# Kernel tuning notes

Hardware: AMD Instinct MI355X
Metric: run time of the kernel (lower is better)

The kernel has to match this reference:

```python
import jax, jax.numpy as jnp
import numpy as np


def setup_inputs() -> dict:
    key = jax.random.key(0)
    ks = jax.random.split(key, 6)
    N, D, B, K, O = 100000, 128, 20000, 32, 128
    features = jax.random.normal(ks[0], (N, D), dtype=jnp.float32)
    raw_features = jax.random.normal(ks[1], (N, D), dtype=jnp.float32)
    W1 = jax.random.normal(ks[2], (D, D), dtype=jnp.float32) * (1.0 / np.sqrt(D))
    b1 = jnp.zeros((D,), dtype=jnp.float32)
    Wn = jax.random.normal(ks[3], (2 * D, O), dtype=jnp.float32) * (1.0 / np.sqrt(2 * D))
    node = jax.random.randint(ks[4], (B, 1), 0, N, dtype=jnp.int64)
    neighbours = jax.random.randint(ks[5], (B, K), 0, N, dtype=jnp.int64)
    return {"features": features, "raw_features": raw_features, "W1": W1,
            "b1": b1, "Wn": Wn, "node": node, "neighbours": neighbours}


def reference(features, raw_features, W1, b1, Wn, node, neighbours):
    # Gather self and neighbor features (irregular access)
    node_feat = features[node[:, 0]]            # [B, D]
    neigh_feat = features[neighbours]           # [B, K, D]
    # Dense + relu applied per neighbor (the single dense layer in build())
    h = jax.nn.relu(jnp.einsum('bkd,de->bke', neigh_feat, W1) + b1)  # [B, K, D]
    # meanpooling over neighbors
    pooled = jnp.mean(h, axis=1)                # [B, D]
    # concat + matmul + relu activation
    out = jax.nn.relu(jnp.concatenate([node_feat, pooled], axis=-1) @ Wn)  # [B, O]
    return (out, raw_features)
```

## Files before the change

### kernel.cpp

```cpp
#include <hip/hip_runtime.h>
#include <hip/hip_bf16.h>
#include <stdint.h>

typedef __bf16 bf16x8 __attribute__((ext_vector_type(8)));
typedef float  f32x4  __attribute__((ext_vector_type(4)));
typedef float  f32x2  __attribute__((ext_vector_type(2)));

#define N_NODES 100000
#define DIM     128
#define B_BATCH 20000
#define K_NB    32
#define O_OUT   128

#define GLOAD16(g, l)  __builtin_amdgcn_global_load_lds(                        \
    (const __attribute__((address_space(1))) void*)(g),                         \
    (__attribute__((address_space(3))) void*)(l), 16, 0, 0)

__device__ inline float blo(uint32_t u) { return __uint_as_float(u << 16); }
__device__ inline float bhi(uint32_t u) { return __uint_as_float(u & 0xffff0000u); }

__global__ void prep_weights(const float* __restrict__ W1,
                             const float* __restrict__ Wn,
                             __bf16* __restrict__ W1f,
                             __bf16* __restrict__ Wnf) {
    int tid = blockIdx.x * blockDim.x + threadIdx.x;
    if (tid < 16384) {
        int e = tid & 7, l = (tid >> 3) & 63, ct = (tid >> 9) & 7, kt = tid >> 12;
        int r0 = l & 15, kg = l >> 4;
        W1f[tid] = (__bf16)W1[(kt * 32 + kg * 8 + e) * DIM + ct * 16 + r0];
    }
    int t2 = tid - 16384;
    if (t2 >= 0 && t2 < 32768) {
        int e = t2 & 7, l = (t2 >> 3) & 63, ct = (t2 >> 9) & 7, kt = t2 >> 12;
        int r0 = l & 15, kg = l >> 4;
        Wnf[t2] = (__bf16)Wn[(kt * 32 + kg * 8 + e) * O_OUT + ct * 16 + r0];
    }
}

__global__ __launch_bounds__(256, 2)
void gemm_h(const float* __restrict__ X, const __bf16* __restrict__ W1f,
            const float* __restrict__ b1, __bf16* __restrict__ H) {
    __shared__ char lds[65536];
    char* Xs = lds;
    char* Wf = lds + 32768;
    const int tid = threadIdx.x;
    const int lane = tid & 63, wave = tid >> 6;
    const int r0 = lane & 15, kg = lane >> 4;
    const long base = (long)blockIdx.x * 64;

#pragma unroll
    for (int i = 0; i < 8; ++i) {
        int chunk = i * 256 + wave * 64 + lane;
        int lrow = chunk >> 5;
        int coff = (chunk & 31) << 4;
        long grow = base + lrow; if (grow > N_NODES - 1) grow = N_NODES - 1;
        const char* g = (const char*)X + grow * 512 + (coff ^ ((lrow & 7) << 4));
        GLOAD16(g, Xs + chunk * 16);
    }
#pragma unroll
    for (int i = 0; i < 8; ++i) {
        int chunk = i * 256 + wave * 64 + lane;
        GLOAD16((const char*)W1f + chunk * 16, Wf + chunk * 16);
    }
    __syncthreads();

    f32x4 acc[8];
#pragma unroll
    for (int t = 0; t < 8; ++t) acc[t] = (f32x4)0.0f;

    const int row = wave * 16 + r0;
    const int swz = (r0 & 7) << 4;
#pragma unroll
    for (int kt = 0; kt < 4; ++kt) {
        const int c0 = kt * 128 + kg * 32;
        f32x4 a0 = *(const f32x4*)(Xs + row * 512 + (c0 ^ swz));
        f32x4 a1 = *(const f32x4*)(Xs + row * 512 + ((c0 + 16) ^ swz));
        bf16x8 af;
        af[0]=(__bf16)a0[0]; af[1]=(__bf16)a0[1]; af[2]=(__bf16)a0[2]; af[3]=(__bf16)a0[3];
        af[4]=(__bf16)a1[0]; af[5]=(__bf16)a1[1]; af[6]=(__bf16)a1[2]; af[7]=(__bf16)a1[3];
#pragma unroll
        for (int ct = 0; ct < 8; ++ct) {
            bf16x8 bf = *(const bf16x8*)(Wf + ((kt * 8 + ct) * 64 + lane) * 16);
            acc[ct] = __builtin_amdgcn_mfma_f32_16x16x32_bf16(af, bf, acc[ct], 0, 0, 0);
        }
    }

    const long orow_base = base + wave * 16 + kg * 4;
#pragma unroll
    for (int ct = 0; ct < 8; ++ct) {
        const int col = ct * 16 + r0;
        const float bias = b1[col];
#pragma unroll
        for (int r = 0; r < 4; ++r) {
            const long orow = orow_base + r;
            if (orow < N_NODES) {
                float v = acc[ct][r] + bias;
                H[orow * DIM + col] = (__bf16)(v > 0.f ? v : 0.f);
            }
        }
    }
}

__global__ __launch_bounds__(256)
void pool_concat(const __bf16* __restrict__ H, const float* __restrict__ X,
                 const int* __restrict__ node, const int* __restrict__ nb,
                 __bf16* __restrict__ Cc) {
    const int lane = threadIdx.x & 63, wave = threadIdx.x >> 6;
    const int b = blockIdx.x * 4 + wave;
    const int g = lane >> 4, c = lane & 15;
    const int swz = (b & 7) << 4;
    char* crow = (char*)Cc + (long)b * 512;

    const int ni = node[b];
    f32x2 nf = *(const f32x2*)(X + (long)ni * DIM + lane * 2);
    union { __bf16 h[2]; uint32_t u; } pk;
    pk.h[0] = (__bf16)nf[0]; pk.h[1] = (__bf16)nf[1];
    *(uint32_t*)(crow + ((lane * 4) ^ swz)) = pk.u;

    const int* nbp = nb + b * K_NB;
    int idx[8];
#pragma unroll
    for (int i = 0; i < 8; ++i) idx[i] = nbp[i * 4 + g];
    float s[8] = {0.f, 0.f, 0.f, 0.f, 0.f, 0.f, 0.f, 0.f};
#pragma unroll
    for (int i = 0; i < 8; ++i) {
        uint4 u = *(const uint4*)(H + (long)idx[i] * DIM + c * 8);
        s[0] += blo(u.x); s[1] += bhi(u.x);
        s[2] += blo(u.y); s[3] += bhi(u.y);
        s[4] += blo(u.z); s[5] += bhi(u.z);
        s[6] += blo(u.w); s[7] += bhi(u.w);
    }
#pragma unroll
    for (int e = 0; e < 8; ++e) {
        s[e] += __shfl_xor(s[e], 16);
        s[e] += __shfl_xor(s[e], 32);
    }
    if (g == 0) {
        union { __bf16 h[8]; uint4 u; } pq;
#pragma unroll
        for (int e = 0; e < 8; ++e) pq.h[e] = (__bf16)(s[e] * (1.0f / K_NB));
        *(uint4*)(crow + ((256 + c * 16) ^ swz)) = pq.u;
    }
}

__global__ __launch_bounds__(256, 2)
void gemm_out(const __bf16* __restrict__ Cc, const __bf16* __restrict__ Wnf,
              float* __restrict__ Out) {
    __shared__ char lds[65536];
    char* As = lds;
    char* Wb = lds + 32768;
    const int tid = threadIdx.x;
    const int lane = tid & 63, wave = tid >> 6;
    const int r0 = lane & 15, kg = lane >> 4;
    const long base = (long)blockIdx.x * 64;

#pragma unroll
    for (int i = 0; i < 8; ++i) {
        int chunk = i * 256 + wave * 64 + lane;
        int lrow = chunk >> 5;
        long grow = base + lrow; if (grow > B_BATCH - 1) grow = B_BATCH - 1;
        const char* g = (const char*)Cc + grow * 512 + ((chunk & 31) << 4);
        GLOAD16(g, As + chunk * 16);
    }
#pragma unroll
    for (int i = 0; i < 8; ++i) {
        int chunk = i * 256 + wave * 64 + lane;
        GLOAD16((const char*)Wnf + chunk * 16, Wb + chunk * 16);
    }
    __syncthreads();

    f32x4 acc[8];
#pragma unroll
    for (int t = 0; t < 8; ++t) acc[t] = (f32x4)0.0f;

    const int row = wave * 16 + r0;
    const int swz = (r0 & 7) << 4;
#pragma unroll
    for (int kt = 0; kt < 4; ++kt) {
        bf16x8 af = *(const bf16x8*)(As + row * 512 + ((kt * 64 + kg * 16) ^ swz));
#pragma unroll
        for (int ct = 0; ct < 8; ++ct) {
            bf16x8 bf = *(const bf16x8*)(Wb + ((kt * 8 + ct) * 64 + lane) * 16);
            acc[ct] = __builtin_amdgcn_mfma_f32_16x16x32_bf16(af, bf, acc[ct], 0, 0, 0);
        }
    }
    __syncthreads();
#pragma unroll
    for (int i = 0; i < 8; ++i) {
        int chunk = i * 256 + wave * 64 + lane;
        GLOAD16((const char*)Wnf + 32768 + chunk * 16, Wb + chunk * 16);
    }
    __syncthreads();
#pragma unroll
    for (int kt = 4; kt < 8; ++kt) {
        bf16x8 af = *(const bf16x8*)(As + row * 512 + ((kt * 64 + kg * 16) ^ swz));
#pragma unroll
        for (int ct = 0; ct < 8; ++ct) {
            bf16x8 bf = *(const bf16x8*)(Wb + (((kt - 4) * 8 + ct) * 64 + lane) * 16);
            acc[ct] = __builtin_amdgcn_mfma_f32_16x16x32_bf16(af, bf, acc[ct], 0, 0, 0);
        }
    }

    const long orow_base = base + wave * 16 + kg * 4;
#pragma unroll
    for (int ct = 0; ct < 8; ++ct) {
        const int col = ct * 16 + r0;
#pragma unroll
        for (int r = 0; r < 4; ++r) {
            const long orow = orow_base + r;
            if (orow < B_BATCH) {
                float v = acc[ct][r];
                Out[orow * O_OUT + col] = v > 0.f ? v : 0.f;
            }
        }
    }
}

__global__ __launch_bounds__(256)
void copy_raw(const float4* __restrict__ src, float4* __restrict__ dst, int n4) {
    int i = blockIdx.x * blockDim.x + threadIdx.x;
    const int stride = gridDim.x * blockDim.x;
    for (; i < n4; i += stride) dst[i] = src[i];
}

extern "C" void kernel_launch(void* const* d_in, const int* in_sizes, int n_in,
                              void* d_out, int out_size, void* d_ws, size_t ws_size,
                              hipStream_t stream) {
    const float* features = (const float*)d_in[0];
    const float* raw      = (const float*)d_in[1];
    const float* W1       = (const float*)d_in[2];
    const float* b1       = (const float*)d_in[3];
    const float* Wn       = (const float*)d_in[4];
    const int*   node     = (const int*)d_in[5];
    const int*   nb       = (const int*)d_in[6];
    float* out = (float*)d_out;

    char* ws = (char*)d_ws;
    __bf16* H   = (__bf16*)ws;
    __bf16* W1f = (__bf16*)(ws + 25600000);
    __bf16* Wnf = (__bf16*)(ws + 25632768);
    __bf16* Cc  = (__bf16*)(ws + 25698304);

    prep_weights<<<192, 256, 0, stream>>>(W1, Wn, W1f, Wnf);
    gemm_h<<<(N_NODES + 63) / 64, 256, 0, stream>>>(features, W1f, b1, H);
    pool_concat<<<B_BATCH / 4, 256, 0, stream>>>(H, features, node, nb, Cc);
    gemm_out<<<(B_BATCH + 63) / 64, 256, 0, stream>>>(Cc, Wnf, out);
    copy_raw<<<2048, 256, 0, stream>>>((const float4*)raw,
                                       (float4*)(out + (long)B_BATCH * O_OUT),
                                       N_NODES * DIM / 4);
}
```

Baseline: 208.1 us.

## Make GEMM kernels persistent with double-buffered LDS tile staging

Both GEMM kernels become persistent: a fixed grid loops over 32-row tiles, loading weights into LDS once per block. The next tile's activations are prefetched into a second LDS buffer with a counted vmcnt wait, so loads overlap the current tile's MFMA work and stores. gemm_out now keeps all 256x128 weights resident (96KB LDS, one block per CU), which removes the mid-kernel weight reload. Each wave now covers half the columns of a 16-row slab. The cost is lower occupancy and the reliance on a hand-counted vmcnt.

Result: faster. 192.3 us (-7.6%).

```diff
diff --git a/kernel.cpp b/kernel.cpp
--- a/kernel.cpp
+++ b/kernel.cpp
@@ -37,67 +37,96 @@
     }
 }
 
+__device__ inline void stage_x(const float* X, long tbase, char* dst, int tid) {
+#pragma unroll
+    for (int i = 0; i < 4; ++i) {
+        int c = tid + i * 256;
+        int lrow = c >> 5;
+        int coff = (c & 31) << 4;
+        const char* g = (const char*)X + (tbase + lrow) * 512 + (coff ^ ((lrow & 7) << 4));
+        GLOAD16(g, dst + c * 16);
+    }
+}
+
+__device__ inline void stage_c(const __bf16* Cc, long tbase, char* dst, int tid) {
+#pragma unroll
+    for (int i = 0; i < 4; ++i) {
+        int c = tid + i * 256;
+        int lrow = c >> 5;
+        const char* g = (const char*)Cc + (tbase + lrow) * 512 + ((c & 31) << 4);
+        GLOAD16(g, dst + c * 16);
+    }
+}
+
 __global__ __launch_bounds__(256, 2)
 void gemm_h(const float* __restrict__ X, const __bf16* __restrict__ W1f,
             const float* __restrict__ b1, __bf16* __restrict__ H) {
     __shared__ char lds[65536];
-    char* Xs = lds;
     char* Wf = lds + 32768;
     const int tid = threadIdx.x;
     const int lane = tid & 63, wave = tid >> 6;
     const int r0 = lane & 15, kg = lane >> 4;
-    const long base = (long)blockIdx.x * 64;
+    const int rbase = (wave & 1) * 16;
+    const int ctbase = (wave >> 1) * 4;
+    const int row = rbase + r0;
+    const int swz = (r0 & 7) << 4;
+    const int NT = N_NODES / 32;
+    const int NB = gridDim.x;
+
+    float bias[4];
+#pragma unroll
+    for (int c = 0; c < 4; ++c) bias[c] = b1[(ctbase + c) * 16 + r0];
 
 #pragma unroll
     for (int i = 0; i < 8; ++i) {
-        int chunk = i * 256 + wave * 64 + lane;
-        int lrow = chunk >> 5;
-        int coff = (chunk & 31) << 4;
-        long grow = base + lrow; if (grow > N_NODES - 1) grow = N_NODES - 1;
-        const char* g = (const char*)X + grow * 512 + (coff ^ ((lrow & 7) << 4));
-        GLOAD16(g, Xs + chunk * 16);
-    }
-#pragma unroll
-    for (int i = 0; i < 8; ++i) {
-        int chunk = i * 256 + wave * 64 + lane;
-        GLOAD16((const char*)W1f + chunk * 16, Wf + chunk * 16);
-    }
-    __syncthreads();
-
-    f32x4 acc[8];
-#pragma unroll
-    for (int t = 0; t < 8; ++t) acc[t] = (f32x4)0.0f;
-
-    const int row = wave * 16 + r0;
-    const int swz = (r0 & 7) << 4;
-#pragma unroll
-    for (int kt = 0; kt < 4; ++kt) {
-        const int c0 = kt * 128 + kg * 32;
-        f32x4 a0 = *(const f32x4*)(Xs + row * 512 + (c0 ^ swz));
-        f32x4 a1 = *(const f32x4*)(Xs + row * 512 + ((c0 + 16) ^ swz));
-        bf16x8 af;
-        af[0]=(__bf16)a0[0]; af[1]=(__bf16)a0[1]; af[2]=(__bf16)a0[2]; af[3]=(__bf16)a0[3];
-        af[4]=(__bf16)a1[0]; af[5]=(__bf16)a1[1]; af[6]=(__bf16)a1[2]; af[7]=(__bf16)a1[3];
-#pragma unroll
-        for (int ct = 0; ct < 8; ++ct) {
-            bf16x8 bf = *(const bf16x8*)(Wf + ((kt * 8 + ct) * 64 + lane) * 16);
-            acc[ct] = __builtin_amdgcn_mfma_f32_16x16x32_bf16(af, bf, acc[ct], 0, 0, 0);
-        }
-    }
-
-    const long orow_base = base + wave * 16 + kg * 4;
-#pragma unroll
-    for (int ct = 0; ct < 8; ++ct) {
-        const int col = ct * 16 + r0;
-        const float bias = b1[col];
-#pragma unroll
-        for (int r = 0; r < 4; ++r) {
-            const long orow = orow_base + r;
-            if (orow < N_NODES) {
-                float v = acc[ct][r] + bias;
-                H[orow * DIM + col] = (__bf16)(v > 0.f ? v : 0.f);
-            }
-        }
+        int c = tid + i * 256;
+        GLOAD16((const char*)W1f + c * 16, Wf + c * 16);
+    }
+    int t = blockIdx.x;
+    char* cur = lds;
+    char* nxt = lds + 16384;
+    stage_x(X, (long)t * 32, cur, tid);
+    asm volatile("s_waitcnt vmcnt(0)" ::: "memory");
+    __builtin_amdgcn_s_barrier();
+
+    while (t < NT) {
+        const int tn = t + NB;
+        if (tn < NT) {
+            stage_x(X, (long)tn * 32, nxt, tid);
+            asm volatile("" ::: "memory");
+        }
+        f32x4 acc[4];
+#pragma unroll
+        for (int i = 0; i < 4; ++i) acc[i] = (f32x4)0.0f;
+#pragma unroll
+        for (int kt = 0; kt < 4; ++kt) {
+            const int c0 = kt * 128 + kg * 32;
+            f32x4 a0 = *(const f32x4*)(cur + row * 512 + (c0 ^ swz));
+            f32x4 a1 = *(const f32x4*)(cur + row * 512 + ((c0 + 16) ^ swz));
+            bf16x8 af;
+            af[0]=(__bf16)a0[0]; af[1]=(__bf16)a0[1]; af[2]=(__bf16)a0[2]; af[3]=(__bf16)a0[3];
+            af[4]=(__bf16)a1[0]; af[5]=(__bf16)a1[1]; af[6]=(__bf16)a1[2]; af[7]=(__bf16)a1[3];
+#pragma unroll
+            for (int cq = 0; cq < 4; ++cq) {
+                bf16x8 bf = *(const bf16x8*)(Wf + ((kt * 8 + ctbase + cq) * 64 + lane) * 16);
+                acc[cq] = __builtin_amdgcn_mfma_f32_16x16x32_bf16(af, bf, acc[cq], 0, 0, 0);
+            }
+        }
+        __bf16* hp = H + ((long)t * 32 + rbase + kg * 4) * DIM + r0;
+#pragma unroll
+        for (int cq = 0; cq < 4; ++cq) {
+#pragma unroll
+            for (int r = 0; r < 4; ++r) {
+                float v = acc[cq][r] + bias[cq];
+                hp[(long)r * DIM + (ctbase + cq) * 16] = (__bf16)(v > 0.f ? v : 0.f);
+            }
+        }
+        if (tn < NT) {
+            asm volatile("s_waitcnt vmcnt(16)" ::: "memory");
+            __builtin_amdgcn_s_barrier();
+        }
+        char* tmp = cur; cur = nxt; nxt = tmp;
+        t = tn;
     }
 }
 
@@ -143,76 +172,66 @@
     }
 }
 
-__global__ __launch_bounds__(256, 2)
+__global__ __launch_bounds__(256, 1)
 void gemm_out(const __bf16* __restrict__ Cc, const __bf16* __restrict__ Wnf,
               float* __restrict__ Out) {
-    __shared__ char lds[65536];
-    char* As = lds;
-    char* Wb = lds + 32768;
+    __shared__ char lds[98304];
+    char* Wf = lds + 32768;
     const int tid = threadIdx.x;
     const int lane = tid & 63, wave = tid >> 6;
     const int r0 = lane & 15, kg = lane >> 4;
-    const long base = (long)blockIdx.x * 64;
-
-#pragma unroll
-    for (int i = 0; i < 8; ++i) {
-        int chunk = i * 256 + wave * 64 + lane;
-        int lrow = chunk >> 5;
-        long grow = base + lrow; if (grow > B_BATCH - 1) grow = B_BATCH - 1;
-        const char* g = (const char*)Cc + grow * 512 + ((chunk & 31) << 4);
-        GLOAD16(g, As + chunk * 16);
-    }
-#pragma unroll
-    for (int i = 0; i < 8; ++i) {
-        int chunk = i * 256 + wave * 64 + lane;
-        GLOAD16((const char*)Wnf + chunk * 16, Wb + chunk * 16);
-    }
-    __syncthreads();
-
-    f32x4 acc[8];
-#pragma unroll
-    for (int t = 0; t < 8; ++t) acc[t] = (f32x4)0.0f;
-
-    const int row = wave * 16 + r0;
+    const int rbase = (wave & 1) * 16;
+    const int ctbase = (wave >> 1) * 4;
+    const int row = rbase + r0;
     const int swz = (r0 & 7) << 4;
-#pragma unroll
-    for (int kt = 0; kt < 4; ++kt) {
-        bf16x8 af = *(const bf16x8*)(As + row * 512 + ((kt * 64 + kg * 16) ^ swz));
-#pragma unroll
-        for (int ct = 0; ct < 8; ++ct) {
-            bf16x8 bf = *(const bf16x8*)(Wb + ((kt * 8 + ct) * 64 + lane) * 16);
-            acc[ct] = __builtin_amdgcn_mfma_f32_16x16x32_bf16(af, bf, acc[ct], 0, 0, 0);
-        }
-    }
-    __syncthreads();
-#pragma unroll
-    for (int i = 0; i < 8; ++i) {
-        int chunk = i * 256 + wave * 64 + lane;
-        GLOAD16((const char*)Wnf + 32768 + chunk * 16, Wb + chunk * 16);
-    }
-    __syncthreads();
-#pragma unroll
-    for (int kt = 4; kt < 8; ++kt) {
-        bf16x8 af = *(const bf16x8*)(As + row * 512 + ((kt * 64 + kg * 16) ^ swz));
-#pragma unroll
-        for (int ct = 0; ct < 8; ++ct) {
-            bf16x8 bf = *(const bf16x8*)(Wb + (((kt - 4) * 8 + ct) * 64 + lane) * 16);
-            acc[ct] = __builtin_amdgcn_mfma_f32_16x16x32_bf16(af, bf, acc[ct], 0, 0, 0);
-        }
-    }
-
-    const long orow_base = base + wave * 16 + kg * 4;
-#pragma unroll
-    for (int ct = 0; ct < 8; ++ct) {
-        const int col = ct * 16 + r0;
-#pragma unroll
-        for (int r = 0; r < 4; ++r) {
-            const long orow = orow_base + r;
-            if (orow < B_BATCH) {
-                float v = acc[ct][r];
-                Out[orow * O_OUT + col] = v > 0.f ? v : 0.f;
-            }
-        }
+    const int NT = B_BATCH / 32;
+    const int NB = gridDim.x;
+
+#pragma unroll
+    for (int i = 0; i < 16; ++i) {
+        int c = tid + i * 256;
+        GLOAD16((const char*)Wnf + c * 16, Wf + c * 16);
+    }
+    int t = blockIdx.x;
+    char* cur = lds;
+    char* nxt = lds + 16384;
+    stage_c(Cc, (long)t * 32, cur, tid);
+    asm volatile("s_waitcnt vmcnt(0)" ::: "memory");
+    __builtin_amdgcn_s_barrier();
+
+    while (t < NT) {
+        const int tn = t + NB;
+        if (tn < NT) {
+            stage_c(Cc, (long)tn * 32, nxt, tid);
+            asm volatile("" ::: "memory");
+        }
+        f32x4 acc[4];
+#pragma unroll
+        for (int i = 0; i < 4; ++i) acc[i] = (f32x4)0.0f;
+#pragma unroll
+        for (int kt = 0; kt < 8; ++kt) {
+            bf16x8 af = *(const bf16x8*)(cur + row * 512 + ((kt * 64 + kg * 16) ^ swz));
+#pragma unroll
+            for (int cq = 0; cq < 4; ++cq) {
+                bf16x8 bf = *(const bf16x8*)(Wf + ((kt * 8 + ctbase + cq) * 64 + lane) * 16);
+                acc[cq] = __builtin_amdgcn_mfma_f32_16x16x32_bf16(af, bf, acc[cq], 0, 0, 0);
+            }
+        }
+        float* op = Out + ((long)t * 32 + rbase + kg * 4) * O_OUT + r0;
+#pragma unroll
+        for (int cq = 0; cq < 4; ++cq) {
+#pragma unroll
+            for (int r = 0; r < 4; ++r) {
+                float v = acc[cq][r];
+                op[(long)r * O_OUT + (ctbase + cq) * 16] = v > 0.f ? v : 0.f;
+            }
+        }
+        if (tn < NT) {
+            asm volatile("s_waitcnt vmcnt(16)" ::: "memory");
+            __builtin_amdgcn_s_barrier();
+        }
+        char* tmp = cur; cur = nxt; nxt = tmp;
+        t = tn;
     }
 }
 
@@ -242,9 +261,9 @@
     __bf16* Cc  = (__bf16*)(ws + 25698304);
 
     prep_weights<<<192, 256, 0, stream>>>(W1, Wn, W1f, Wnf);
-    gemm_h<<<(N_NODES + 63) / 64, 256, 0, stream>>>(features, W1f, b1, H);
+    gemm_h<<<512, 256, 0, stream>>>(features, W1f, b1, H);
     pool_concat<<<B_BATCH / 4, 256, 0, stream>>>(H, features, node, nb, Cc);
-    gemm_out<<<(B_BATCH + 63) / 64, 256, 0, stream>>>(Cc, Wnf, out);
+    gemm_out<<<256, 256, 0, stream>>>(Cc, Wnf, out);
     copy_raw<<<2048, 256, 0, stream>>>((const float4*)raw,
                                        (float4*)(out + (long)B_BATCH * O_OUT),
                                        N_NODES * DIM / 4);
```
